# Performance work log

Measured on AMD Instinct MI355X. Metric: run time of the kernel, lower is better.

The kernel has to match this reference:

```python
import jax, jax.numpy as jnp
import numpy as np

I, H, O, L = 128, 1024, 128, 2

def _linear_init(key, out_f, in_f, bias):
    b = 1.0 / np.sqrt(in_f)
    kw, kb = jax.random.split(key)
    W = jax.random.uniform(kw, (out_f, in_f), jnp.float32, -b, b)
    if bias:
        return W, jax.random.uniform(kb, (out_f,), jnp.float32, -b, b)
    return W, None

def setup_inputs() -> dict:
    key = jax.random.key(0)
    ks = jax.random.split(key, 32)
    inp = {
        'x': jax.random.normal(ks[0], (32, 512, I), jnp.float32),
        'h0': jnp.zeros((32, L, H), jnp.float32),
    }
    ki = 1
    in_dim = I
    for l in range(L):
        Wxz, _ = _linear_init(ks[ki], H, in_dim, False); ki += 1
        Whz, bz = _linear_init(ks[ki], H, H, True); ki += 1
        Wxr, _ = _linear_init(ks[ki], H, in_dim, False); ki += 1
        Whr, br = _linear_init(ks[ki], H, H, True); ki += 1
        Wxg, _ = _linear_init(ks[ki], H, in_dim, False); ki += 1
        Whg, bg = _linear_init(ks[ki], H, H, True); ki += 1
        inp.update({f'Wxz{l}': Wxz, f'Whz{l}': Whz, f'bz{l}': bz,
                    f'Wxr{l}': Wxr, f'Whr{l}': Whr, f'br{l}': br,
                    f'Wxg{l}': Wxg, f'Whg{l}': Whg, f'bg{l}': bg})
        in_dim = H
    Wy, by = _linear_init(ks[ki], O, H, True)
    inp['Wy'] = Wy
    inp['by'] = by
    return inp

def _gru_layer(x_seq, h0, Wxz, Whz, bz, Wxr, Whr, br, Wxg, Whg, bg):
    # Precompute all input projections as big GEMMs (B,S,H)
    xz = jnp.einsum('bsi,hi->bsh', x_seq, Wxz)
    xr = jnp.einsum('bsi,hi->bsh', x_seq, Wxr)
    xg = jnp.einsum('bsi,hi->bsh', x_seq, Wxg)
    def step(h, gates):
        gz, gr, gg = gates
        z = jax.nn.sigmoid(gz + h @ Whz.T + bz)
        r = jax.nn.sigmoid(gr + h @ Whr.T + br)
        g = jnp.tanh(gg + (r * h) @ Whg.T + bg)
        h_new = z * h + (1.0 - z) * g
        return h_new, h_new
    # scan over time: (S,B,H)
    hT, hs = jax.lax.scan(step, h0, (xz.transpose(1, 0, 2), xr.transpose(1, 0, 2), xg.transpose(1, 0, 2)))
    return hs.transpose(1, 0, 2), hT

def reference(x, h0,
              Wxz0, Whz0, bz0, Wxr0, Whr0, br0, Wxg0, Whg0, bg0,
              Wxz1, Whz1, bz1, Wxr1, Whr1, br1, Wxg1, Whg1, bg1,
              Wy, by):
    layers = [
        (Wxz0, Whz0, bz0, Wxr0, Whr0, br0, Wxg0, Whg0, bg0),
        (Wxz1, Whz1, bz1, Wxr1, Whr1, br1, Wxg1, Whg1, bg1),
    ]
    seq = x
    finals = []
    for l, p in enumerate(layers):
        seq, hT = _gru_layer(seq, h0[:, l, :], *p)
        finals.append(hT)
    y = jnp.einsum('bsh,oh->bso', seq, Wy) + by  # (B,S,O)
    hidden = jnp.stack(finals, axis=1)  # (B,L,H)
    return y, hidden
```

## Files before the change

### kernel.cpp

```cpp
#include <hip/hip_runtime.h>

typedef unsigned short u16;
typedef unsigned int u32;
typedef unsigned long long u64;
typedef __bf16 bf16x8 __attribute__((ext_vector_type(8)));
typedef float f32x4 __attribute__((ext_vector_type(4)));

union FU { f32x4 f; bf16x8 h; };

__device__ __forceinline__ u16 f2b(float f) {
  unsigned u = __float_as_uint(f);
  return (u16)((u + 0x7fffu + ((u >> 16) & 1u)) >> 16);
}

__device__ __forceinline__ void st_b16_llc(u16* p, u16 v) {
  __hip_atomic_store(p, v, __ATOMIC_RELAXED, __HIP_MEMORY_SCOPE_AGENT);
}

__device__ __forceinline__ void st_u32_cc(u32* p, u32 v) {
  asm volatile("global_store_dword %0, %1, off sc0 sc1" :: "v"(p), "v"(v) : "memory");
}

__device__ __forceinline__ u32 ld_dword_cc(const u32* p) {
  u32 v;
  asm volatile("global_load_dword %0, %1, off sc0 sc1\n\ts_waitcnt vmcnt(0)"
               : "=v"(v) : "v"(p) : "memory");
  return v;
}

#define ISSUE8CC(D, P)                                                       \
  asm volatile(                                                              \
      "global_load_dwordx4 %0, %8, off sc0 sc1\n\t"                          \
      "global_load_dwordx4 %1, %8, off offset:64 sc0 sc1\n\t"                \
      "global_load_dwordx4 %2, %8, off offset:128 sc0 sc1\n\t"               \
      "global_load_dwordx4 %3, %8, off offset:192 sc0 sc1\n\t"               \
      "global_load_dwordx4 %4, %8, off offset:256 sc0 sc1\n\t"               \
      "global_load_dwordx4 %5, %8, off offset:320 sc0 sc1\n\t"               \
      "global_load_dwordx4 %6, %8, off offset:384 sc0 sc1\n\t"               \
      "global_load_dwordx4 %7, %8, off offset:448 sc0 sc1"                   \
      : "=&v"((D)[0].f), "=&v"((D)[1].f), "=&v"((D)[2].f), "=&v"((D)[3].f),  \
        "=&v"((D)[4].f), "=&v"((D)[5].f), "=&v"((D)[6].f), "=&v"((D)[7].f)   \
      : "v"(P) : "memory")

#define ISSUE4C(D, P)                                                        \
  asm volatile(                                                              \
      "global_load_dwordx4 %0, %4, off\n\t"                                  \
      "global_load_dwordx4 %1, %4, off offset:64\n\t"                        \
      "global_load_dwordx4 %2, %4, off offset:128\n\t"                       \
      "global_load_dwordx4 %3, %4, off offset:192"                           \
      : "=&v"((D)[0].f), "=&v"((D)[1].f), "=&v"((D)[2].f), "=&v"((D)[3].f)   \
      : "v"(P) : "memory")

#define WAITV(N)                                                             \
  do {                                                                       \
    asm volatile("s_waitcnt vmcnt(" #N ")" ::: "memory");                    \
    __builtin_amdgcn_sched_barrier(0);                                       \
  } while (0)

#define MFMA8ZR(ACC, BUF, KSB)                                               \
  do {                                                                       \
    _Pragma("unroll") for (int j_ = 0; j_ < 8; ++j_)                         \
        ACC = __builtin_amdgcn_mfma_f32_16x16x32_bf16(                       \
            (BUF)[j_].h,                                                     \
            *(const bf16x8*)&zr_frag[(KSB + j_) * 512 + lane * 8],           \
            ACC, 0, 0, 0);                                                   \
  } while (0)
#define MFMA8G(ACC, BUF, KSB)                                                \
  do {                                                                       \
    _Pragma("unroll") for (int j_ = 0; j_ < 8; ++j_)                         \
        ACC = __builtin_amdgcn_mfma_f32_16x16x32_bf16(                       \
            (BUF)[j_].h,                                                     \
            *(const bf16x8*)&g_frag[(KSB + j_) * 256 + boff],                \
            ACC, 0, 0, 0);                                                   \
  } while (0)

__global__ void cast_f32_bf16(const float* __restrict__ in, u16* __restrict__ out, int n) {
  int i = blockIdx.x * 256 + threadIdx.x;
  if (i < n) out[i] = f2b(in[i]);
}

__global__ __launch_bounds__(256) void gemm_bt(
    const u16* __restrict__ A, const u16* __restrict__ B,
    int M, int N, int K,
    const float* __restrict__ bias, float* __restrict__ Cf)
{
  __shared__ u16 a_sm[128 * 32];
  __shared__ u16 b_sm[128 * 32];
  const int tid = threadIdx.x;
  const int lane = tid & 63;
  const int wid = tid >> 6;
  const int wm = wid >> 1, wn = wid & 1;
  const int m0 = blockIdx.x * 128, n0 = blockIdx.y * 128;
  const int q = lane >> 4, l15 = lane & 15, l3 = lane & 3;

  f32x4 acc[4][4];
  #pragma unroll
  for (int i = 0; i < 4; ++i)
    #pragma unroll
    for (int j = 0; j < 4; ++j) acc[i][j] = (f32x4){0.f, 0.f, 0.f, 0.f};

  for (int kk = 0; kk < K; kk += 32) {
    __syncthreads();
    #pragma unroll
    for (int p = 0; p < 2; ++p) {
      int idx = p * 256 + tid;
      int r = idx >> 2, cch = idx & 3;
      *(uint4*)&a_sm[r * 32 + ((cch ^ (r & 3)) * 8)] =
          *(const uint4*)&A[(size_t)(m0 + r) * K + kk + cch * 8];
      *(uint4*)&b_sm[r * 32 + ((cch ^ (r & 3)) * 8)] =
          *(const uint4*)&B[(size_t)(n0 + r) * K + kk + cch * 8];
    }
    __syncthreads();
    bf16x8 af[4], bfr[4];
    #pragma unroll
    for (int s = 0; s < 4; ++s) {
      int ra = wm * 64 + s * 16 + l15;
      af[s] = *(const bf16x8*)&a_sm[ra * 32 + ((q ^ l3) * 8)];
      int rb = wn * 64 + s * 16 + l15;
      bfr[s] = *(const bf16x8*)&b_sm[rb * 32 + ((q ^ l3) * 8)];
    }
    #pragma unroll
    for (int si = 0; si < 4; ++si)
      #pragma unroll
      for (int sj = 0; sj < 4; ++sj)
        acc[si][sj] = __builtin_amdgcn_mfma_f32_16x16x32_bf16(af[si], bfr[sj], acc[si][sj], 0, 0, 0);
  }

  #pragma unroll
  for (int si = 0; si < 4; ++si)
    #pragma unroll
    for (int sj = 0; sj < 4; ++sj)
      #pragma unroll
      for (int e = 0; e < 4; ++e) {
        int m = m0 + wm * 64 + si * 16 + q * 4 + e;
        int n = n0 + wn * 64 + sj * 16 + l15;
        Cf[(size_t)m * N + n] = acc[si][sj][e] + (bias ? bias[n] : 0.f);
      }
}

__global__ __launch_bounds__(192, 1) void gru_pipe(
    const u16* __restrict__ Wh0, const u16* __restrict__ Wx0,
    const u16* __restrict__ Wh1, const u16* __restrict__ Wx1,
    const float* __restrict__ bz0, const float* __restrict__ br0, const float* __restrict__ bg0,
    const float* __restrict__ bz1, const float* __restrict__ br1, const float* __restrict__ bg1,
    const u16* __restrict__ xb,
    const float* __restrict__ h0p,
    u16* __restrict__ h0buf,
    u16* __restrict__ hb1,
    u16* __restrict__ rh0b, u16* __restrict__ rh1b,
    u16* __restrict__ seq1,
    float* __restrict__ hid,
    u32* __restrict__ slots)
{
  __shared__ u16 zr_frag[64 * 512];
  __shared__ u16 g_frag[64 * 256];

  const int tid = threadIdx.x;
  const int lane = tid & 63;
  const int w = tid >> 6;
  const int bid = blockIdx.x;
  u32* lflags = slots + 512;

  const bool Lyr1 = bid >= 128;
  const int nb = (bid & 127) * 8;
  const int q = lane >> 4, c15 = lane & 15, nl = c15 & 7;
  const int n_own = nb + nl;
  const bool isz = c15 < 8;
  const int brow = w * 16 + c15;
  const int boff = (q * 8 + nl) * 8;
  const int aoff = brow * 1024 + q * 8;
  const int KS = Lyr1 ? 64 : 36;
  const int IN = Lyr1 ? 1024 : 128;
  const u16* Wh = Lyr1 ? Wh1 : Wh0;
  const u16* Wx = Lyr1 ? Wx1 : Wx0;
  const size_t WXG = (size_t)1024 * IN;

  const int d_own = (Lyr1 ? 2 : 0) | (w & 1);
  const int d_oth = (Lyr1 ? 0 : 2) | (w & 1);
  u32* slot_ptr = &slots[d_own * 128 + (bid & 127)];
  const int rrep = bid >> 5;
  const bool laneOth = (lane & 1) != 0;
  const u32* lfp = &lflags[rrep * 32 + (laneOth ? d_oth : d_own)];

  float hreg[4], zreg[4] = {0.f, 0.f, 0.f, 0.f};

  if (tid < 128) {
    for (int cidx = tid; cidx < KS * 64; cidx += 128) {
      int ks = cidx >> 6, l = cidx & 63;
      int lq = l >> 4, lc = l & 15;
      int row = nb + (lc & 7), gate = (lc < 8) ? 0 : 1;
      int k0 = ks * 32 + lq * 8;
      const u16* src = (k0 < 1024)
          ? Wh + (size_t)gate * 1048576 + (size_t)row * 1024 + k0
          : Wx + (size_t)gate * WXG + (size_t)row * IN + (k0 - 1024);
      *(uint4*)&zr_frag[cidx * 8] = *(const uint4*)src;
    }
    for (int gidx = tid; gidx < KS * 32; gidx += 128) {
      int ks = gidx >> 5, s = gidx & 31;
      int lq = s >> 3, r8 = s & 7;
      int row = nb + r8, k0 = ks * 32 + lq * 8;
      const u16* src = (k0 < 1024)
          ? Wh + (size_t)2 * 1048576 + (size_t)row * 1024 + k0
          : Wx + (size_t)2 * WXG + (size_t)row * IN + (k0 - 1024);
      *(uint4*)&g_frag[gidx * 8] = *(const uint4*)src;
    }
    #pragma unroll
    for (int e = 0; e < 4; ++e) {
      int b = w * 16 + q * 4 + e;
      float v = h0p[b * 2048 + (Lyr1 ? 1024 : 0) + n_own];
      hreg[e] = v;
      if (isz)
        st_b16_llc((Lyr1 ? hb1 : h0buf + 32768) + b * 1024 + n_own, f2b(v));
    }
  }
  __syncthreads();

  if (w == 2) {
    if (bid == 0) {
      const u32* my = slots + lane * 8;
      const int dgrp = lane >> 4;
      u32 pub = 0;
      for (;;) {
        uint4 va, vb;
        asm volatile(
            "global_load_dwordx4 %0, %2, off sc0 sc1\n\t"
            "global_load_dwordx4 %1, %2, off offset:16 sc0 sc1\n\t"
            "s_waitcnt vmcnt(0)"
            : "=&v"(va), "=&v"(vb) : "v"(my) : "memory");
        u32 m = min(min(min(va.x, va.y), min(va.z, va.w)),
                    min(min(vb.x, vb.y), min(vb.z, vb.w)));
        m = min(m, (u32)__shfl_xor((int)m, 1));
        m = min(m, (u32)__shfl_xor((int)m, 2));
        m = min(m, (u32)__shfl_xor((int)m, 4));
        m = min(m, (u32)__shfl_xor((int)m, 8));
        if (m > pub) {
          pub = m;
          if ((lane & 15) == 0) {
            #pragma unroll
            for (int r = 0; r < 8; ++r) st_u32_cc(&lflags[r * 32 + dgrp], m);
          }
        }
        if (__all(pub >= 1026u)) break;
        __builtin_amdgcn_s_sleep(1);
      }
    }
    return;
  }

  if (lane == 0) st_u32_cc(slot_ptr, 1u);

  const float bias1 = isz ? (Lyr1 ? bz1 : bz0)[n_own] : (Lyr1 ? br1 : br0)[n_own];
  const float bias2 = (Lyr1 ? bg1 : bg0)[n_own];

  FU xfu[4];
  FU sA[8], sB[8], sC[8];

  for (int p = 0; p < 1026; ++p) {
    const int t = p >> 1, ph = p & 1;

    {
      const u32 tgt = laneOth ? ((Lyr1 && ph == 0) ? (u32)(p + 1) : (u32)p)
                              : (u32)(p + 1);
      for (;;) {
        u32 v = ld_dword_cc(lfp);
        if (__all(v >= tgt)) break;
        __builtin_amdgcn_s_sleep(1);
      }
    }

    if (!Lyr1) {
      if (t < 512) {
        f32x4 a0 = {0.f,0.f,0.f,0.f}, a1 = {0.f,0.f,0.f,0.f};
        if (ph == 0) {
          const u16* hp = h0buf + ((t - 1) & 1) * 32768 + aoff;
          const u16* xp = xb + ((size_t)brow * 512 + t) * 128 + q * 8;
          ISSUE4C(xfu, xp);
          ISSUE8CC(sA, hp);
          ISSUE8CC(sB, hp + 256);
          ISSUE8CC(sC, hp + 512);
          WAITV(16); MFMA8ZR(a0, sA, 0);
          ISSUE8CC(sA, hp + 768);
          WAITV(16); MFMA8ZR(a0, sB, 8);
          WAITV(8);  MFMA8ZR(a0, sC, 16);
          WAITV(0);  MFMA8ZR(a0, sA, 24);
          #pragma unroll
          for (int j = 0; j < 4; ++j)
            a1 = __builtin_amdgcn_mfma_f32_16x16x32_bf16(
                xfu[j].h, *(const bf16x8*)&zr_frag[(32 + j) * 512 + lane * 8], a1, 0, 0, 0);
          float hsh[4];
          #pragma unroll
          for (int e = 0; e < 4; ++e) hsh[e] = __shfl_xor(hreg[e], 8);
          #pragma unroll
          for (int e = 0; e < 4; ++e) {
            float pre = a0[e] + a1[e] + bias1;
            float s = 1.f / (1.f + __expf(-pre));
            if (isz) zreg[e] = s;
            else st_b16_llc(&rh0b[(w * 16 + q * 4 + e) * 1024 + n_own], f2b(s * hsh[e]));
          }
        } else {
          const u16* rp = rh0b + aoff;
          ISSUE8CC(sA, rp);
          ISSUE8CC(sB, rp + 256);
          ISSUE8CC(sC, rp + 512);
          WAITV(16); MFMA8G(a0, sA, 0);
          ISSUE8CC(sA, rp + 768);
          WAITV(16); MFMA8G(a0, sB, 8);
          WAITV(8);  MFMA8G(a0, sC, 16);
          WAITV(0);  MFMA8G(a0, sA, 24);
          #pragma unroll
          for (int j = 0; j < 4; ++j)
            a1 = __builtin_amdgcn_mfma_f32_16x16x32_bf16(
                xfu[j].h, *(const bf16x8*)&g_frag[(32 + j) * 256 + boff], a1, 0, 0, 0);
          if (isz) {
            u16* hout = h0buf + (t & 1) * 32768;
            #pragma unroll
            for (int e = 0; e < 4; ++e) {
              int b = w * 16 + q * 4 + e;
              float pre = a0[e] + a1[e] + bias2;
              float ex = __expf(2.f * pre);
              float gv = 1.f - 2.f / (ex + 1.f);
              float hn = zreg[e] * hreg[e] + (1.f - zreg[e]) * gv;
              hreg[e] = hn;
              st_b16_llc(&hout[b * 1024 + n_own], f2b(hn));
              if (t == 511) hid[b * 2048 + n_own] = hn;
            }
          }
        }
      }
    } else {
      if (t >= 1) {
        const int s = t - 1;
        f32x4 a0 = {0.f,0.f,0.f,0.f}, a1 = {0.f,0.f,0.f,0.f};
        const u16* hp = h0buf + (s & 1) * 32768 + aoff;
        if (ph == 0) {
          const u16* hb = hb1 + aoff;
          ISSUE8CC(sA, hb);
          ISSUE8CC(sB, hb + 256);
          ISSUE8CC(sC, hb + 512);
          WAITV(16); MFMA8ZR(a0, sA, 0);  ISSUE8CC(sA, hb + 768);
          WAITV(16); MFMA8ZR(a0, sB, 8);  ISSUE8CC(sB, hp);
          WAITV(16); MFMA8ZR(a0, sC, 16); ISSUE8CC(sC, hp + 256);
          WAITV(16); MFMA8ZR(a0, sA, 24); ISSUE8CC(sA, hp + 512);
          WAITV(16); MFMA8ZR(a1, sB, 32); ISSUE8CC(sB, hp + 768);
          WAITV(16); MFMA8ZR(a1, sC, 40);
          WAITV(8);  MFMA8ZR(a1, sA, 48);
          WAITV(0);  MFMA8ZR(a1, sB, 56);
          float hsh[4];
          #pragma unroll
          for (int e = 0; e < 4; ++e) hsh[e] = __shfl_xor(hreg[e], 8);
          #pragma unroll
          for (int e = 0; e < 4; ++e) {
            float pre = a0[e] + a1[e] + bias1;
            float sg = 1.f / (1.f + __expf(-pre));
            if (isz) zreg[e] = sg;
            else st_b16_llc(&rh1b[(w * 16 + q * 4 + e) * 1024 + n_own], f2b(sg * hsh[e]));
          }
        } else {
          const u16* rp = rh1b + aoff;
          ISSUE8CC(sA, rp);
          ISSUE8CC(sB, rp + 256);
          ISSUE8CC(sC, rp + 512);
          WAITV(16); MFMA8G(a0, sA, 0);  ISSUE8CC(sA, rp + 768);
          WAITV(16); MFMA8G(a0, sB, 8);  ISSUE8CC(sB, hp);
          WAITV(16); MFMA8G(a0, sC, 16); ISSUE8CC(sC, hp + 256);
          WAITV(16); MFMA8G(a0, sA, 24); ISSUE8CC(sA, hp + 512);
          WAITV(16); MFMA8G(a1, sB, 32); ISSUE8CC(sB, hp + 768);
          WAITV(16); MFMA8G(a1, sC, 40);
          WAITV(8);  MFMA8G(a1, sA, 48);
          WAITV(0);  MFMA8G(a1, sB, 56);
          if (isz) {
            #pragma unroll
            for (int e = 0; e < 4; ++e) {
              int b = w * 16 + q * 4 + e;
              float pre = a0[e] + a1[e] + bias2;
              float ex = __expf(2.f * pre);
              float gv = 1.f - 2.f / (ex + 1.f);
              float hn = zreg[e] * hreg[e] + (1.f - zreg[e]) * gv;
              hreg[e] = hn;
              u16 hnb = f2b(hn);
              st_b16_llc(&hb1[b * 1024 + n_own], hnb);
              seq1[((size_t)b * 512 + s) * 1024 + n_own] = hnb;
              if (s == 511) hid[1024 + b * 2048 + n_own] = hn;
            }
          }
        }
      }
    }

    if (p < 1025) {
      WAITV(0);
      if (lane == 0) st_u32_cc(slot_ptr, (u32)(p + 2));
    }
  }
}

extern "C" void kernel_launch(void* const* d_in, const int* in_sizes, int n_in,
                              void* d_out, int out_size, void* d_ws, size_t ws_size,
                              hipStream_t stream) {
  (void)in_sizes; (void)n_in; (void)out_size; (void)ws_size;
  char* ws = (char*)d_ws;
  const size_t MB = 1024ull * 1024ull;
  u16* seq1 = (u16*)(ws + 0);
  u16* xb   = (u16*)(ws + 32 * MB);
  u16* Wh0  = (u16*)(ws + 36 * MB);
  u16* Wh1  = (u16*)(ws + 42 * MB);
  u16* Wx0  = (u16*)(ws + 48 * MB);
  u16* Wx1  = (u16*)(ws + 49 * MB);
  u16* Wyb  = (u16*)(ws + 55 * MB);
  u16* h0buf = (u16*)(ws + 56 * MB);
  u16* hb1  = (u16*)(ws + 56 * MB + 128 * 1024);
  u16* rh0b = (u16*)(ws + 56 * MB + 192 * 1024);
  u16* rh1b = (u16*)(ws + 56 * MB + 256 * 1024);
  u32* slots = (u32*)(ws + 56 * MB + 320 * 1024);

  hipMemsetAsync(slots, 0, 4096, stream);

  auto cast = [&](const void* in, u16* out, int n) {
    cast_f32_bf16<<<(n + 255) / 256, 256, 0, stream>>>((const float*)in, out, n);
  };
  cast(d_in[0], xb, 2097152);
  cast(d_in[3],  Wh0 + 0,       1048576);
  cast(d_in[6],  Wh0 + 1048576, 1048576);
  cast(d_in[9],  Wh0 + 2097152, 1048576);
  cast(d_in[12], Wh1 + 0,       1048576);
  cast(d_in[15], Wh1 + 1048576, 1048576);
  cast(d_in[18], Wh1 + 2097152, 1048576);
  cast(d_in[2],  Wx0 + 0,      131072);
  cast(d_in[5],  Wx0 + 131072, 131072);
  cast(d_in[8],  Wx0 + 262144, 131072);
  cast(d_in[11], Wx1 + 0,       1048576);
  cast(d_in[14], Wx1 + 1048576, 1048576);
  cast(d_in[17], Wx1 + 2097152, 1048576);
  cast(d_in[20], Wyb, 131072);

  float* y_out = (float*)d_out;
  float* hid = y_out + 2097152;

  gru_pipe<<<256, dim3(192), 0, stream>>>(
      Wh0, Wx0, Wh1, Wx1,
      (const float*)d_in[4],  (const float*)d_in[7],  (const float*)d_in[10],
      (const float*)d_in[13], (const float*)d_in[16], (const float*)d_in[19],
      xb, (const float*)d_in[1],
      h0buf, hb1, rh0b, rh1b, seq1, hid, slots);

  gemm_bt<<<dim3(128, 1), dim3(256), 0, stream>>>(
      seq1, Wyb, 16384, 128, 1024, (const float*)d_in[21], y_out);
}
```

Baseline: 6.712 ms.

## Pack bf16 stores via shuffles and reuse layer-1 x-part gate MFMA across phases

Each lane's 16-bit stores of r*h, h, and seq1 outputs are gathered with two xor-shuffles into 64-bit values, and one lane in four writes them with a single coherent dwordx2 store. This cuts the number of narrow coherent stores on the per-step critical path. In layer 1, the input-projection part of the candidate gate (from the layer-0 h) is now computed in phase 0 alongside the z/r MFMAs and carried into phase 1. Phase 1 then loads only the r*h operand, halving its dependent global loads. This adds extra MFMAs and registers to phase 0 and relies on the lane-to-column mapping for correct packing.

New measurement: 6.117 ms (median of 2 runs). 8.9% less time.

```diff
diff --git a/kernel.cpp b/kernel.cpp
--- a/kernel.cpp
+++ b/kernel.cpp
@@ -20,12 +20,20 @@
 __device__ __forceinline__ void st_u32_cc(u32* p, u32 v) {
   asm volatile("global_store_dword %0, %1, off sc0 sc1" :: "v"(p), "v"(v) : "memory");
 }
+__device__ __forceinline__ void st_u64_cc(void* p, u64 v) {
+  asm volatile("global_store_dwordx2 %0, %1, off sc0 sc1" :: "v"(p), "v"(v) : "memory");
+}
 
 __device__ __forceinline__ u32 ld_dword_cc(const u32* p) {
   u32 v;
   asm volatile("global_load_dword %0, %1, off sc0 sc1\n\ts_waitcnt vmcnt(0)"
                : "=v"(v) : "v"(p) : "memory");
   return v;
+}
+
+__device__ __forceinline__ u64 pack4(u32 lo) {
+  u32 p2 = lo | ((u32)__shfl_xor((int)lo, 1) << 16);
+  return (u64)p2 | ((u64)(u32)__shfl_xor((int)p2, 2) << 32);
 }
 
 #define ISSUE8CC(D, P)                                                       \
@@ -183,6 +191,7 @@
   const u32* lfp = &lflags[rrep * 32 + (laneOth ? d_oth : d_own)];
 
   float hreg[4], zreg[4] = {0.f, 0.f, 0.f, 0.f};
+  f32x4 a1g = {0.f, 0.f, 0.f, 0.f};
 
   if (tid < 128) {
     for (int cidx = tid; cidx < KS * 64; cidx += 128) {
@@ -295,7 +304,11 @@
             float pre = a0[e] + a1[e] + bias1;
             float s = 1.f / (1.f + __expf(-pre));
             if (isz) zreg[e] = s;
-            else st_b16_llc(&rh0b[(w * 16 + q * 4 + e) * 1024 + n_own], f2b(s * hsh[e]));
+            else {
+              u64 p4 = pack4((u32)f2b(s * hsh[e]));
+              if ((c15 & 3) == 0)
+                st_u64_cc(&rh0b[(w * 16 + q * 4 + e) * 1024 + nb + (c15 & 7)], p4);
+            }
           }
         } else {
           const u16* rp = rh0b + aoff;
@@ -321,7 +334,8 @@
               float gv = 1.f - 2.f / (ex + 1.f);
               float hn = zreg[e] * hreg[e] + (1.f - zreg[e]) * gv;
               hreg[e] = hn;
-              st_b16_llc(&hout[b * 1024 + n_own], f2b(hn));
+              u64 p4 = pack4((u32)f2b(hn));
+              if ((c15 & 3) == 0) st_u64_cc(&hout[b * 1024 + nb + c15], p4);
               if (t == 511) hid[b * 2048 + n_own] = hn;
             }
           }
@@ -331,9 +345,10 @@
       if (t >= 1) {
         const int s = t - 1;
         f32x4 a0 = {0.f,0.f,0.f,0.f}, a1 = {0.f,0.f,0.f,0.f};
-        const u16* hp = h0buf + (s & 1) * 32768 + aoff;
         if (ph == 0) {
+          const u16* hp = h0buf + (s & 1) * 32768 + aoff;
           const u16* hb = hb1 + aoff;
+          a1g = (f32x4){0.f, 0.f, 0.f, 0.f};
           ISSUE8CC(sA, hb);
           ISSUE8CC(sB, hb + 256);
           ISSUE8CC(sC, hb + 512);
@@ -341,10 +356,11 @@
           WAITV(16); MFMA8ZR(a0, sB, 8);  ISSUE8CC(sB, hp);
           WAITV(16); MFMA8ZR(a0, sC, 16); ISSUE8CC(sC, hp + 256);
           WAITV(16); MFMA8ZR(a0, sA, 24); ISSUE8CC(sA, hp + 512);
-          WAITV(16); MFMA8ZR(a1, sB, 32); ISSUE8CC(sB, hp + 768);
-          WAITV(16); MFMA8ZR(a1, sC, 40);
-          WAITV(8);  MFMA8ZR(a1, sA, 48);
-          WAITV(0);  MFMA8ZR(a1, sB, 56);
+          WAITV(16); MFMA8ZR(a1, sB, 32); MFMA8G(a1g, sB, 32);
+                     ISSUE8CC(sB, hp + 768);
+          WAITV(16); MFMA8ZR(a1, sC, 40); MFMA8G(a1g, sC, 40);
+          WAITV(8);  MFMA8ZR(a1, sA, 48); MFMA8G(a1g, sA, 48);
+          WAITV(0);  MFMA8ZR(a1, sB, 56); MFMA8G(a1g, sB, 56);
           float hsh[4];
           #pragma unroll
           for (int e = 0; e < 4; ++e) hsh[e] = __shfl_xor(hreg[e], 8);
@@ -353,33 +369,36 @@
             float pre = a0[e] + a1[e] + bias1;
             float sg = 1.f / (1.f + __expf(-pre));
             if (isz) zreg[e] = sg;
-            else st_b16_llc(&rh1b[(w * 16 + q * 4 + e) * 1024 + n_own], f2b(sg * hsh[e]));
+            else {
+              u64 p4 = pack4((u32)f2b(sg * hsh[e]));
+              if ((c15 & 3) == 0)
+                st_u64_cc(&rh1b[(w * 16 + q * 4 + e) * 1024 + nb + (c15 & 7)], p4);
+            }
           }
         } else {
           const u16* rp = rh1b + aoff;
           ISSUE8CC(sA, rp);
           ISSUE8CC(sB, rp + 256);
           ISSUE8CC(sC, rp + 512);
-          WAITV(16); MFMA8G(a0, sA, 0);  ISSUE8CC(sA, rp + 768);
-          WAITV(16); MFMA8G(a0, sB, 8);  ISSUE8CC(sB, hp);
-          WAITV(16); MFMA8G(a0, sC, 16); ISSUE8CC(sC, hp + 256);
-          WAITV(16); MFMA8G(a0, sA, 24); ISSUE8CC(sA, hp + 512);
-          WAITV(16); MFMA8G(a1, sB, 32); ISSUE8CC(sB, hp + 768);
-          WAITV(16); MFMA8G(a1, sC, 40);
-          WAITV(8);  MFMA8G(a1, sA, 48);
-          WAITV(0);  MFMA8G(a1, sB, 56);
+          WAITV(16); MFMA8G(a0, sA, 0);
+          ISSUE8CC(sA, rp + 768);
+          WAITV(16); MFMA8G(a0, sB, 8);
+          WAITV(8);  MFMA8G(a0, sC, 16);
+          WAITV(0);  MFMA8G(a0, sA, 24);
           if (isz) {
             #pragma unroll
             for (int e = 0; e < 4; ++e) {
               int b = w * 16 + q * 4 + e;
-              float pre = a0[e] + a1[e] + bias2;
+              float pre = a0[e] + a1g[e] + bias2;
               float ex = __expf(2.f * pre);
               float gv = 1.f - 2.f / (ex + 1.f);
               float hn = zreg[e] * hreg[e] + (1.f - zreg[e]) * gv;
               hreg[e] = hn;
-              u16 hnb = f2b(hn);
-              st_b16_llc(&hb1[b * 1024 + n_own], hnb);
-              seq1[((size_t)b * 512 + s) * 1024 + n_own] = hnb;
+              u64 p4 = pack4((u32)f2b(hn));
+              if ((c15 & 3) == 0) {
+                st_u64_cc(&hb1[b * 1024 + nb + c15], p4);
+                *(u64*)&seq1[((size_t)b * 512 + s) * 1024 + nb + c15] = p4;
+              }
               if (s == 511) hid[1024 + b * 2048 + n_own] = hn;
             }
           }
```
